# Optimization experiments

Hardware: AMD Instinct MI355X
Metric: run time of the kernel (lower is better)

Reference implementation:

```python
import jax, jax.numpy as jnp
import numpy as np

# Complex-YOLO / YOLOv2 anchors (anchor_step = 2)
ANCHORS = np.array([1.08, 1.19, 3.42, 4.41, 6.63, 11.38, 9.42, 5.11, 16.62, 10.52], np.float32).reshape(5, 2)
NA = 5          # num_anchors
NC = 8          # num_classes
COORD_SCALE = 1.0
NOOBJECT_SCALE = 1.0
OBJECT_SCALE = 10.0
CLASS_SCALE = 1.0
SIL_THRESH = 0.6

B, H, W, T = 32, 32, 64, 50


def setup_inputs() -> dict:
    key = jax.random.key(0)
    k1, k2 = jax.random.split(key)
    output = jax.random.normal(k1, (B, NA * (7 + NC), H, W), dtype=jnp.float32)
    # target layout: (cls, x, y, w, l, im, re), normalized coords in (0,1); col 1 != 0 => valid box
    target = jax.random.uniform(k2, (B, T, 7), dtype=jnp.float32, minval=0.01, maxval=1.0)
    return {"output": output, "target": target}


def _iou_cxcywh(b1, b2):
    # b1, b2: (..., 4) as (cx, cy, w, h); axis-aligned IoU, matching bbox_ious(x1y1x2y2=False)
    mx = jnp.minimum(b1[..., 0] - b1[..., 2] / 2, b2[..., 0] - b2[..., 2] / 2)
    Mx = jnp.maximum(b1[..., 0] + b1[..., 2] / 2, b2[..., 0] + b2[..., 2] / 2)
    my = jnp.minimum(b1[..., 1] - b1[..., 3] / 2, b2[..., 1] - b2[..., 3] / 2)
    My = jnp.maximum(b1[..., 1] + b1[..., 3] / 2, b2[..., 1] + b2[..., 3] / 2)
    cw = b1[..., 2] + b2[..., 2] - (Mx - mx)
    ch = b1[..., 3] + b2[..., 3] - (My - my)
    inter = jnp.where((cw > 0) & (ch > 0), cw * ch, 0.0)
    union = b1[..., 2] * b1[..., 3] + b2[..., 2] * b2[..., 3] - inter
    return inter / union


def _region_loss(output, target):
    nB, _, nH, nW = output.shape
    anc = jnp.asarray(ANCHORS)  # [NA, 2]
    out = output.reshape(nB, NA, 7 + NC, nH, nW)
    x = jax.nn.sigmoid(out[:, :, 0])
    y = jax.nn.sigmoid(out[:, :, 1])
    w = out[:, :, 2]
    l = out[:, :, 3]
    im = out[:, :, 4]
    re = out[:, :, 5]
    conf = jax.nn.sigmoid(out[:, :, 6])
    cls_logits = jnp.moveaxis(out[:, :, 7:], 2, -1)  # [B, A, H, W, C]

    # ---- decoded pred boxes (detached, like .data in torch) ----
    sg = jax.lax.stop_gradient
    grid_x = jnp.arange(nW, dtype=jnp.float32)
    grid_y = jnp.arange(nH, dtype=jnp.float32)
    pbx = sg(x) + grid_x[None, None, None, :]
    pby = sg(y) + grid_y[None, None, :, None]
    pbw = jnp.exp(sg(w)) * anc[None, :, 0, None, None]
    pbl = jnp.exp(sg(l)) * anc[None, :, 1, None, None]
    pred = jnp.stack([pbx, pby, pbw, pbl], axis=-1).reshape(nB, NA * nH * nW, 4)  # [B, N, 4]

    # ---- build_targets (fully vectorized) ----
    tgt = sg(target)
    nT = tgt.shape[1]
    valid = jnp.cumprod((tgt[..., 1] != 0).astype(jnp.int32), axis=1).astype(bool)  # break-on-zero semantics
    gx = tgt[..., 1] * nW
    gy = tgt[..., 2] * nH
    gw = tgt[..., 3] * nW
    gl = tgt[..., 4] * nH
    gi = jnp.clip(gx.astype(jnp.int32), 0, nW - 1)
    gj = jnp.clip(gy.astype(jnp.int32), 0, nH - 1)
    gt = jnp.stack([gx, gy, gw, gl], axis=-1)  # [B, T, 4]

    # IoU of every pred box against every GT -> silence mask
    ious = _iou_cxcywh(gt[:, :, None, :], pred[:, None, :, :])  # [B, T, N]
    ious = jnp.where(valid[..., None], ious, 0.0)
    max_iou = ious.max(axis=1)  # [B, N]
    conf_mask = jnp.where(max_iou > SIL_THRESH, 0.0, NOOBJECT_SCALE).reshape(nB, NA, nH, nW)

    # anchor matching: IoU of (0,0,gw,gl) vs (0,0,aw,ah) -> closed form
    inter_a = jnp.minimum(gw[..., None], anc[None, None, :, 0]) * jnp.minimum(gl[..., None], anc[None, None, :, 1])
    union_a = (gw * gl)[..., None] + (anc[:, 0] * anc[:, 1])[None, None, :] - inter_a
    a_iou = inter_a / union_a  # [B, T, A]
    best_n = jnp.argmax(a_iou, axis=-1)
    aw = anc[best_n, 0]
    al = anc[best_n, 1]

    # winner cell per GT; later GTs overwrite earlier ones at the same cell (torch loop order)
    b_idx = jnp.arange(nB)[:, None]
    lin = ((b_idx * NA + best_n) * nH + gj) * nW + gi  # [B, T]
    M = nB * NA * nH * nW
    t_eff = jnp.where(valid, jnp.arange(nT)[None, :], -1)
    seg = jax.ops.segment_max(t_eff.reshape(-1), lin.reshape(-1), num_segments=M)
    keep = valid & (t_eff == seg[lin])
    lin_safe = jnp.where(keep, lin, M).reshape(-1)  # route losers to dummy slot

    def scat(vals):
        return jnp.zeros(M + 1, jnp.float32).at[lin_safe].set(vals.reshape(-1))[:M].reshape(nB, NA, nH, nW)

    cm = scat(keep.astype(jnp.float32))           # coord_mask == cls_mask
    tx = scat(gx - gi)
    ty = scat(gy - gj)
    tw = scat(jnp.log(gw / aw))
    tl = scat(jnp.log(gl / al))
    tim = scat(tgt[..., 5])
    tre = scat(tgt[..., 6])
    tcls = scat(tgt[..., 0]).astype(jnp.int32)

    n_idx = best_n * (nH * nW) + gj * nW + gi
    pb = pred[b_idx, n_idx]                       # [B, T, 4] pred box at winner cell
    tconf = scat(_iou_cxcywh(gt, pb))
    conf_mask = jnp.where(cm > 0, OBJECT_SCALE, conf_mask)

    # ---- masked losses ----
    def mse(p, t):
        return jnp.sum((p * cm - t * cm) ** 2)

    loss_x = COORD_SCALE * mse(x, tx)
    loss_y = COORD_SCALE * mse(y, ty)
    loss_w = COORD_SCALE * mse(w, tw)
    loss_l = COORD_SCALE * mse(l, tl)
    loss_im = COORD_SCALE * mse(im, tim)
    loss_re = COORD_SCALE * mse(re, tre)
    loss_conf = jnp.sum((conf * conf_mask - tconf * conf_mask) ** 2)
    ce = jax.nn.logsumexp(cls_logits, axis=-1) - jnp.take_along_axis(cls_logits, tcls[..., None], axis=-1)[..., 0]
    loss_cls = CLASS_SCALE * jnp.sum(cm * ce)
    return loss_x + loss_y + loss_w + loss_l + loss_conf + loss_cls + loss_im + loss_re


def reference(output, target):
    return _region_loss(output, target)
```

## Files before the change

### kernel.cpp

```cpp
#include <hip/hip_runtime.h>
#include <math.h>

#define NB 32
#define NA 5
#define NC 8
#define NH 32
#define NW 64
#define NT 50
#define NCH (7 + NC)
#define HW (NH * NW)
#define OBJECT_SCALE 10.0f

__constant__ float c_anchors[NA * 2] = {
    1.08f, 1.19f, 3.42f, 4.41f, 6.63f, 11.38f, 9.42f, 5.11f, 16.62f, 10.52f};

__device__ __forceinline__ float fast_exp(float v) { return __expf(v); }
__device__ __forceinline__ float fast_log(float v) { return __logf(v); }
__device__ __forceinline__ float fast_sigmoid(float v) {
    return __builtin_amdgcn_rcpf(1.0f + __expf(-v));
}

__global__ void prep_kernel(const float* __restrict__ target,
                            int* __restrict__ nvalid,
                            float* __restrict__ tA,
                            float* __restrict__ tB,
                            float* __restrict__ out) {
    int b = blockIdx.x;
    int t = threadIdx.x;
    const float* tp = target + (size_t)(b * NT + t) * 7;

    float t0 = 0.f, t1 = 0.f, t2 = 0.f, t3 = 0.f, t4 = 0.f, t5 = 0.f, t6 = 0.f;
    if (t < NT) {
        t0 = tp[0]; t1 = tp[1]; t2 = tp[2]; t3 = tp[3];
        t4 = tp[4]; t5 = tp[5]; t6 = tp[6];
    }
    unsigned long long bal = __ballot(t < NT && t1 != 0.0f);
    if (t == 0) {
        int nv = __ffsll((unsigned long long)~bal) - 1;
        nvalid[b] = nv;
        if (b == 0) out[0] = 0.0f;
    }
    if (t >= NT) return;

    float gx = t1 * (float)NW;
    float gy = t2 * (float)NH;
    float gw = t3 * (float)NW;
    float gl = t4 * (float)NH;

    int best_n = 0;
    float best = -1.0f;
#pragma unroll
    for (int a = 0; a < NA; ++a) {
        float aw = c_anchors[2 * a], al = c_anchors[2 * a + 1];
        float inter = fminf(gw, aw) * fminf(gl, al);
        float uni = gw * gl + aw * al - inter;
        float iou = inter / uni;
        if (iou > best) { best = iou; best_n = a; }
    }
    float aw = c_anchors[2 * best_n], al = c_anchors[2 * best_n + 1];

    int gi = min(max((int)gx, 0), NW - 1);
    int gj = min(max((int)gy, 0), NH - 1);

    float area = gw * gl;
    float* a8 = tA + (size_t)(b * NT + t) * 8;
    a8[0] = gx - gw * 0.5f;
    a8[1] = gx + gw * 0.5f;
    a8[2] = gy - gl * 0.5f;
    a8[3] = gy + gl * 0.5f;
    a8[4] = 0.375f * area;
    a8[5] = (float)((best_n << 12) | (gj << 6) | gi);
    a8[6] = 0.f;
    a8[7] = 0.f;

    float* b8 = tB + (size_t)(b * NT + t) * 8;
    b8[0] = gx - (float)gi;
    b8[1] = gy - (float)gj;
    b8[2] = t5;
    b8[3] = t6;
    b8[4] = t0;
    b8[5] = fast_log(gw / aw);
    b8[6] = fast_log(gl / al);
    b8[7] = area;
}

__global__ __launch_bounds__(256) void cell_kernel(const float* __restrict__ output,
                                                   const float* __restrict__ tA,
                                                   const float* __restrict__ tB,
                                                   const int* __restrict__ nvalid,
                                                   float* __restrict__ out) {
    const int blocks_per_b = (NA * HW) / 256;
    int b = blockIdx.x / blocks_per_b;
    int m = (blockIdx.x % blocks_per_b) * 256 + threadIdx.x;
    int a = m >> 11;
    int rem = m & (HW - 1);
    int j = rem >> 6;
    int i = rem & (NW - 1);

    const float* op = output + (size_t)(b * NA + a) * NCH * HW + (j << 6) + i;
    float o0 = op[0 * HW], o1 = op[1 * HW], o2 = op[2 * HW], o3 = op[3 * HW];
    float o6 = op[6 * HW];

    float x = fast_sigmoid(o0);
    float y = fast_sigmoid(o1);
    float conf = fast_sigmoid(o6);

    float aw = c_anchors[2 * a], al = c_anchors[2 * a + 1];
    float pbx = x + (float)i;
    float pby = y + (float)j;
    float pbw = fast_exp(o2) * aw;
    float pbl = fast_exp(o3) * al;

    float plx = pbx - pbw * 0.5f;
    float phx = pbx + pbw * 0.5f;
    float ply = pby - pbl * 0.5f;
    float phy = pby + pbl * 0.5f;
    float parea = pbw * pbl;
    float mycode = (float)((a << 12) | (j << 6) | i);

    int nv = nvalid[b];
    const float* tb8 = tA + (size_t)b * NT * 8;

    float silm = -1e30f;
    int ta = -1;
#pragma unroll 2
    for (int t = 0; t < nv; ++t) {
        const float* ti = tb8 + t * 8;
        float tlx = ti[0], thx = ti[1], tly = ti[2], thy = ti[3];
        float ct2 = ti[4], code = ti[5];
        float cw = fminf(thx, phx) - fmaxf(tlx, plx);
        float ch = fminf(thy, phy) - fmaxf(tly, ply);
        float cwc = fmaxf(cw, 0.0f);
        float chc = fmaxf(ch, 0.0f);
        silm = fmaxf(silm, __builtin_fmaf(cwc, chc, -ct2));
        if (code == mycode) ta = t;
    }

    float loss;
    if (ta >= 0) {
        const float* ai = tb8 + (size_t)ta * 8;
        const float* bi = tB + ((size_t)b * NT + ta) * 8;
        float tlx = ai[0], thx = ai[1], tly = ai[2], thy = ai[3];
        float tarea = bi[7];
        float cw = fminf(thx, phx) - fmaxf(tlx, plx);
        float ch = fminf(thy, phy) - fmaxf(tly, ply);
        float inter = fmaxf(cw, 0.0f) * fmaxf(ch, 0.0f);
        float tconf = inter / (tarea + parea - inter);

        float o4 = op[4 * HW], o5 = op[5 * HW];
        float dx = x - bi[0];
        float dy = y - bi[1];
        float dw = o2 - bi[5];
        float dl = o3 - bi[6];
        float di = o4 - bi[2];
        float dr = o5 - bi[3];
        loss = dx * dx + dy * dy + dw * dw + dl * dl + di * di + dr * dr;

        float dc = OBJECT_SCALE * (conf - tconf);
        loss += dc * dc;

        float cl[NC];
#pragma unroll
        for (int c = 0; c < NC; ++c) cl[c] = op[(size_t)(7 + c) * HW];
        int tcls = min(max((int)bi[4], 0), NC - 1);
        float mxl = cl[0];
#pragma unroll
        for (int c = 1; c < NC; ++c) mxl = fmaxf(mxl, cl[c]);
        float s = 0.0f;
#pragma unroll
        for (int c = 0; c < NC; ++c) s += fast_exp(cl[c] - mxl);
        loss += (mxl + fast_log(s)) - cl[tcls];
    } else {
        bool silenced = silm > 0.375f * parea;
        loss = silenced ? 0.0f : conf * conf;
    }

    for (int off = 32; off > 0; off >>= 1)
        loss += __shfl_down(loss, off, 64);
    __shared__ float s_part[4];
    int wave = threadIdx.x >> 6;
    int lane = threadIdx.x & 63;
    if (lane == 0) s_part[wave] = loss;
    __syncthreads();
    if (threadIdx.x == 0)
        atomicAdd(out, s_part[0] + s_part[1] + s_part[2] + s_part[3]);
}

extern "C" void kernel_launch(void* const* d_in, const int* in_sizes, int n_in,
                              void* d_out, int out_size, void* d_ws, size_t ws_size,
                              hipStream_t stream) {
    const float* output = (const float*)d_in[0];
    const float* target = (const float*)d_in[1];
    float* out = (float*)d_out;
    int* nvalid = (int*)d_ws;
    float* tA = (float*)((char*)d_ws + 128);
    float* tB = tA + (size_t)NB * NT * 8;

    hipLaunchKernelGGL(prep_kernel, dim3(NB), dim3(64), 0, stream,
                       target, nvalid, tA, tB, out);
    hipLaunchKernelGGL(cell_kernel, dim3(NB * 40), dim3(256), 0, stream,
                       output, tA, tB, nvalid, out);
}
```

Before: 88.99 us.

## Fuse target prep into cell kernel with per-block shared-memory target tables

Removes the separate prep kernel. Each block now recomputes the per-batch target table (box bounds, anchor match, regression targets) with its first wave and keeps it in shared memory instead of global workspace. The output is zeroed with a hipMemsetAsync. The target scan loop now reads float4/float2 from LDS and is unrolled 4. This trades one kernel launch and the global round trip for redundant prep work in each of the 40 blocks per batch, plus an extra memset node and a __syncthreads.

```diff
diff --git a/kernel.cpp b/kernel.cpp
--- a/kernel.cpp
+++ b/kernel.cpp
@@ -10,6 +10,7 @@
 #define NCH (7 + NC)
 #define HW (NH * NW)
 #define OBJECT_SCALE 10.0f
+#define BLOCKS_PER_B ((NA * HW) / 256)
 
 __constant__ float c_anchors[NA * 2] = {
     1.08f, 1.19f, 3.42f, 4.41f, 6.63f, 11.38f, 9.42f, 5.11f, 16.62f, 10.52f};
@@ -20,78 +21,71 @@
     return __builtin_amdgcn_rcpf(1.0f + __expf(-v));
 }
 
-__global__ void prep_kernel(const float* __restrict__ target,
-                            int* __restrict__ nvalid,
-                            float* __restrict__ tA,
-                            float* __restrict__ tB,
-                            float* __restrict__ out) {
-    int b = blockIdx.x;
-    int t = threadIdx.x;
-    const float* tp = target + (size_t)(b * NT + t) * 7;
+__global__ __launch_bounds__(256) void fused_kernel(const float* __restrict__ output,
+                                                    const float* __restrict__ target,
+                                                    float* __restrict__ out) {
+    __shared__ __align__(16) float sA[NT * 8];
+    __shared__ __align__(16) float sB[NT * 8];
+    __shared__ int s_nv;
+    __shared__ float s_part[4];
 
-    float t0 = 0.f, t1 = 0.f, t2 = 0.f, t3 = 0.f, t4 = 0.f, t5 = 0.f, t6 = 0.f;
-    if (t < NT) {
-        t0 = tp[0]; t1 = tp[1]; t2 = tp[2]; t3 = tp[3];
-        t4 = tp[4]; t5 = tp[5]; t6 = tp[6];
+    int b = blockIdx.x / BLOCKS_PER_B;
+
+    if (threadIdx.x < 64) {
+        int t = threadIdx.x;
+        const float* tp = target + (size_t)(b * NT + t) * 7;
+        float t0 = 0.f, t1 = 0.f, t2 = 0.f, t3 = 0.f, t4 = 0.f, t5 = 0.f, t6 = 0.f;
+        if (t < NT) {
+            t0 = tp[0]; t1 = tp[1]; t2 = tp[2]; t3 = tp[3];
+            t4 = tp[4]; t5 = tp[5]; t6 = tp[6];
+        }
+        unsigned long long bal = __ballot(t < NT && t1 != 0.0f);
+        if (t == 0) s_nv = __ffsll((unsigned long long)~bal) - 1;
+
+        if (t < NT) {
+            float gx = t1 * (float)NW;
+            float gy = t2 * (float)NH;
+            float gw = t3 * (float)NW;
+            float gl = t4 * (float)NH;
+
+            int best_n = 0;
+            float best = -1.0f;
+#pragma unroll
+            for (int aa = 0; aa < NA; ++aa) {
+                float aw = c_anchors[2 * aa], al = c_anchors[2 * aa + 1];
+                float inter = fminf(gw, aw) * fminf(gl, al);
+                float uni = gw * gl + aw * al - inter;
+                float iou = inter / uni;
+                if (iou > best) { best = iou; best_n = aa; }
+            }
+            float aw = c_anchors[2 * best_n], al = c_anchors[2 * best_n + 1];
+
+            int gi = min(max((int)gx, 0), NW - 1);
+            int gj = min(max((int)gy, 0), NH - 1);
+
+            float area = gw * gl;
+            float* a8 = sA + t * 8;
+            a8[0] = gx - gw * 0.5f;
+            a8[1] = gx + gw * 0.5f;
+            a8[2] = gy - gl * 0.5f;
+            a8[3] = gy + gl * 0.5f;
+            a8[4] = 0.375f * area;
+            a8[5] = (float)((best_n << 12) | (gj << 6) | gi);
+
+            float* b8 = sB + t * 8;
+            b8[0] = gx - (float)gi;
+            b8[1] = gy - (float)gj;
+            b8[2] = t5;
+            b8[3] = t6;
+            b8[4] = t0;
+            b8[5] = fast_log(gw / aw);
+            b8[6] = fast_log(gl / al);
+            b8[7] = area;
+        }
     }
-    unsigned long long bal = __ballot(t < NT && t1 != 0.0f);
-    if (t == 0) {
-        int nv = __ffsll((unsigned long long)~bal) - 1;
-        nvalid[b] = nv;
-        if (b == 0) out[0] = 0.0f;
-    }
-    if (t >= NT) return;
+    __syncthreads();
 
-    float gx = t1 * (float)NW;
-    float gy = t2 * (float)NH;
-    float gw = t3 * (float)NW;
-    float gl = t4 * (float)NH;
-
-    int best_n = 0;
-    float best = -1.0f;
-#pragma unroll
-    for (int a = 0; a < NA; ++a) {
-        float aw = c_anchors[2 * a], al = c_anchors[2 * a + 1];
-        float inter = fminf(gw, aw) * fminf(gl, al);
-        float uni = gw * gl + aw * al - inter;
-        float iou = inter / uni;
-        if (iou > best) { best = iou; best_n = a; }
-    }
-    float aw = c_anchors[2 * best_n], al = c_anchors[2 * best_n + 1];
-
-    int gi = min(max((int)gx, 0), NW - 1);
-    int gj = min(max((int)gy, 0), NH - 1);
-
-    float area = gw * gl;
-    float* a8 = tA + (size_t)(b * NT + t) * 8;
-    a8[0] = gx - gw * 0.5f;
-    a8[1] = gx + gw * 0.5f;
-    a8[2] = gy - gl * 0.5f;
-    a8[3] = gy + gl * 0.5f;
-    a8[4] = 0.375f * area;
-    a8[5] = (float)((best_n << 12) | (gj << 6) | gi);
-    a8[6] = 0.f;
-    a8[7] = 0.f;
-
-    float* b8 = tB + (size_t)(b * NT + t) * 8;
-    b8[0] = gx - (float)gi;
-    b8[1] = gy - (float)gj;
-    b8[2] = t5;
-    b8[3] = t6;
-    b8[4] = t0;
-    b8[5] = fast_log(gw / aw);
-    b8[6] = fast_log(gl / al);
-    b8[7] = area;
-}
-
-__global__ __launch_bounds__(256) void cell_kernel(const float* __restrict__ output,
-                                                   const float* __restrict__ tA,
-                                                   const float* __restrict__ tB,
-                                                   const int* __restrict__ nvalid,
-                                                   float* __restrict__ out) {
-    const int blocks_per_b = (NA * HW) / 256;
-    int b = blockIdx.x / blocks_per_b;
-    int m = (blockIdx.x % blocks_per_b) * 256 + threadIdx.x;
+    int m = (blockIdx.x % BLOCKS_PER_B) * 256 + threadIdx.x;
     int a = m >> 11;
     int rem = m & (HW - 1);
     int j = rem >> 6;
@@ -118,28 +112,26 @@
     float parea = pbw * pbl;
     float mycode = (float)((a << 12) | (j << 6) | i);
 
-    int nv = nvalid[b];
-    const float* tb8 = tA + (size_t)b * NT * 8;
+    int nv = s_nv;
 
     float silm = -1e30f;
     int ta = -1;
-#pragma unroll 2
+#pragma unroll 4
     for (int t = 0; t < nv; ++t) {
-        const float* ti = tb8 + t * 8;
-        float tlx = ti[0], thx = ti[1], tly = ti[2], thy = ti[3];
-        float ct2 = ti[4], code = ti[5];
-        float cw = fminf(thx, phx) - fmaxf(tlx, plx);
-        float ch = fminf(thy, phy) - fmaxf(tly, ply);
+        float4 r0 = *reinterpret_cast<const float4*>(sA + (t << 3));
+        float2 r1 = *reinterpret_cast<const float2*>(sA + (t << 3) + 4);
+        float cw = fminf(r0.y, phx) - fmaxf(r0.x, plx);
+        float ch = fminf(r0.w, phy) - fmaxf(r0.z, ply);
         float cwc = fmaxf(cw, 0.0f);
         float chc = fmaxf(ch, 0.0f);
-        silm = fmaxf(silm, __builtin_fmaf(cwc, chc, -ct2));
-        if (code == mycode) ta = t;
+        silm = fmaxf(silm, __builtin_fmaf(cwc, chc, -r1.x));
+        if (r1.y == mycode) ta = t;
     }
 
     float loss;
     if (ta >= 0) {
-        const float* ai = tb8 + (size_t)ta * 8;
-        const float* bi = tB + ((size_t)b * NT + ta) * 8;
+        const float* ai = sA + (ta << 3);
+        const float* bi = sB + (ta << 3);
         float tlx = ai[0], thx = ai[1], tly = ai[2], thy = ai[3];
         float tarea = bi[7];
         float cw = fminf(thx, phx) - fmaxf(tlx, plx);
@@ -177,7 +169,6 @@
 
     for (int off = 32; off > 0; off >>= 1)
         loss += __shfl_down(loss, off, 64);
-    __shared__ float s_part[4];
     int wave = threadIdx.x >> 6;
     int lane = threadIdx.x & 63;
     if (lane == 0) s_part[wave] = loss;
@@ -192,12 +183,9 @@
     const float* output = (const float*)d_in[0];
     const float* target = (const float*)d_in[1];
     float* out = (float*)d_out;
-    int* nvalid = (int*)d_ws;
-    float* tA = (float*)((char*)d_ws + 128);
-    float* tB = tA + (size_t)NB * NT * 8;
+    (void)d_ws; (void)ws_size;
 
-    hipLaunchKernelGGL(prep_kernel, dim3(NB), dim3(64), 0, stream,
-                       target, nvalid, tA, tB, out);
-    hipLaunchKernelGGL(cell_kernel, dim3(NB * 40), dim3(256), 0, stream,
-                       output, tA, tB, nvalid, out);
+    hipMemsetAsync(d_out, 0, sizeof(float), stream);
+    hipLaunchKernelGGL(fused_kernel, dim3(NB * BLOCKS_PER_B), dim3(256), 0, stream,
+                       output, target, out);
 }
```

Result: faster. 83.44 us (-6.2%).
